# Performance work log

Measured on AMD Instinct MI355X. Metric: run time of the kernel, lower is better.

Reference implementation:

```python
import jax, jax.numpy as jnp
import numpy as np
import math

B, L, DIM = 2, 2048, 2048
N_HEADS, N_KV = 16, 4
HD = DIM // N_HEADS          # 128
N_REP = N_HEADS // N_KV      # 4
THETA = 10000.0


def setup_inputs() -> dict:
    key = jax.random.key(0)
    ks = jax.random.split(key, 6)
    x = jax.random.normal(ks[0], (B, L, DIM), dtype=jnp.float32)
    # rotary phasor freqs_cis = exp(i * t * inv_freq), stored as cos/sin
    inv_freq = 1.0 / (THETA ** (jnp.arange(0, HD, 2, dtype=jnp.float32) / HD))  # [HD//2]
    ang = jnp.arange(L, dtype=jnp.float32)[:, None] * inv_freq[None, :]          # [L, HD//2]
    freqs_cos = jnp.cos(ang)
    freqs_sin = jnp.sin(ang)
    s = 0.02
    wq = jax.random.normal(ks[1], (DIM, DIM), dtype=jnp.float32) * s
    wk = jax.random.normal(ks[2], (N_KV * HD, DIM), dtype=jnp.float32) * s
    wv = jax.random.normal(ks[3], (N_KV * HD, DIM), dtype=jnp.float32) * s
    wo = jax.random.normal(ks[4], (DIM, DIM), dtype=jnp.float32) * s
    return {"x": x, "freqs_cos": freqs_cos, "freqs_sin": freqs_sin,
            "wq": wq, "wk": wk, "wv": wv, "wo": wo}


def _apply_rope(t, cos, sin):
    # t: [B, L, H, HD]; cos/sin: [L, HD//2] -> broadcast [1, L, 1, HD//2]
    tr = t.reshape(*t.shape[:-1], HD // 2, 2)
    t0, t1 = tr[..., 0], tr[..., 1]
    c = cos[None, :, None, :]
    s = sin[None, :, None, :]
    r0 = t0 * c - t1 * s
    r1 = t0 * s + t1 * c
    return jnp.stack([r0, r1], axis=-1).reshape(t.shape)


def reference(x, freqs_cos, freqs_sin, wq, wk, wv, wo):
    Bx, Lx, _ = x.shape
    xq = (x @ wq.T).reshape(Bx, Lx, N_HEADS, HD)
    xk = (x @ wk.T).reshape(Bx, Lx, N_KV, HD)
    xv = (x @ wv.T).reshape(Bx, Lx, N_KV, HD)
    xq = _apply_rope(xq, freqs_cos, freqs_sin)
    xk = _apply_rope(xk, freqs_cos, freqs_sin)
    # repeat_kv (GQA expansion) then [B, H, L, HD]
    keys = jnp.repeat(xk, N_REP, axis=2).transpose(0, 2, 1, 3)
    values = jnp.repeat(xv, N_REP, axis=2).transpose(0, 2, 1, 3)
    q = xq.transpose(0, 2, 1, 3)
    scores = jnp.einsum('bhqd,bhkd->bhqk', q, keys) / math.sqrt(HD)
    mask = jnp.triu(jnp.full((Lx, Lx), -jnp.inf, dtype=scores.dtype), k=1)
    scores = scores + mask[None, None]
    probs = jax.nn.softmax(scores.astype(jnp.float32), axis=-1).astype(q.dtype)
    out = jnp.einsum('bhqk,bhkd->bhqd', probs, values)
    out = out.transpose(0, 2, 1, 3).reshape(Bx, Lx, -1)
    output = out @ wo.T
    return (output, keys, values)
```

## Files before the change

kernel.cpp:

```cpp
#include <hip/hip_runtime.h>
#include <hip/hip_bf16.h>

using bf16x8 = __attribute__((ext_vector_type(8))) short;
using f32x4  = __attribute__((ext_vector_type(4))) float;

__device__ __forceinline__ unsigned short f32_to_bf16(float f) {
  unsigned u = __float_as_uint(f);
  u += 0x7FFFu + ((u >> 16) & 1u);
  return (unsigned short)(u >> 16);
}
__device__ __forceinline__ unsigned pack2(float lo, float hi) {
  __hip_bfloat162 h = __float22bfloat162_rn(make_float2(lo, hi));
  return *reinterpret_cast<unsigned*>(&h);
}
__device__ __forceinline__ void gload_lds16(const void* g, void* l) {
  __builtin_amdgcn_global_load_lds(
      (const __attribute__((address_space(1))) unsigned int*)g,
      (__attribute__((address_space(3))) unsigned int*)l, 16, 0, 0);
}

__global__ void cast_all_kernel(const float* __restrict__ wq, const float* __restrict__ wo,
                                const float* __restrict__ wk, const float* __restrict__ wv,
                                const float* __restrict__ x,
                                unsigned short* __restrict__ WQKV,
                                unsigned short* __restrict__ WO,
                                unsigned short* __restrict__ XBF) {
  int i = blockIdx.x * blockDim.x + threadIdx.x;
  const float4* s; ushort4* d; int j;
  if (i < 1048576)      { s = (const float4*)wq; d = (ushort4*)WQKV;            j = i; }
  else if (i < 2097152) { s = (const float4*)wo; d = (ushort4*)WO;              j = i - 1048576; }
  else if (i < 2359296) { s = (const float4*)wk; d = (ushort4*)WQKV + 1048576;  j = i - 2097152; }
  else if (i < 2621440) { s = (const float4*)wv; d = (ushort4*)WQKV + 1310720;  j = i - 2359296; }
  else                  { s = (const float4*)x;  d = (ushort4*)XBF;             j = i - 2621440; }
  float4 v = s[j];
  ushort4 o;
  o.x = f32_to_bf16(v.x); o.y = f32_to_bf16(v.y);
  o.z = f32_to_bf16(v.z); o.w = f32_to_bf16(v.w);
  d[j] = o;
}

template <int BM, int MODE>
__global__ __launch_bounds__(512, 2) void gemm256_kernel(
    const unsigned short* __restrict__ A, const unsigned short* __restrict__ Bw,
    float* __restrict__ C, unsigned short* __restrict__ qbf_out,
    float* __restrict__ xkv_out, int M, int N, int K) {
  constexpr int ABYTES = BM * 128;
  constexpr int BBYTES = 256 * 128;
  constexpr int BUFB   = ABYTES + BBYTES;
  constexpr int ALOADS = BM / 64;
  constexpr int WROWS  = BM / 32;
  __shared__ __align__(16) char Lsh[2 * BUFB];

  const int tid = threadIdx.x;
  const int wid = tid >> 6, lane = tid & 63;
  const int lr = lane & 15, lg = lane >> 4;
  const int wr = wid >> 2, wc = wid & 3;
  const int bn = blockIdx.x, bm = blockIdx.y;
  const int x0 = lg * 16;

  f32x4 acc[WROWS][4] = {};

  const char* Ag = (const char*)A + (size_t)(bm * BM) * K * 2;
  const char* Bg = (const char*)Bw + (size_t)(bn * 256) * K * 2;

  int aoff[ALOADS], boff[4];
#pragma unroll
  for (int i = 0; i < ALOADS; ++i) {
    int lin = wid * (BM * 16) + i * 1024 + lane * 16;
    int grow = lin >> 7;
    int gcol = (lin & 127) ^ ((grow & 7) << 4);
    aoff[i] = grow * (K * 2) + gcol;
  }
#pragma unroll
  for (int i = 0; i < 4; ++i) {
    int lin = wid * 4096 + i * 1024 + lane * 16;
    int grow = lin >> 7;
    int gcol = (lin & 127) ^ ((grow & 7) << 4);
    boff[i] = grow * (K * 2) + gcol;
  }

  auto stage = [&](int s, int buf) {
    const int kb = s * 128;
    char* Lb = Lsh + buf * BUFB;
#pragma unroll
    for (int i = 0; i < ALOADS; ++i)
      gload_lds16(Ag + aoff[i] + kb, Lb + wid * (BM * 16) + i * 1024);
#pragma unroll
    for (int i = 0; i < 4; ++i)
      gload_lds16(Bg + boff[i] + kb, Lb + ABYTES + wid * 4096 + i * 1024);
  };

  auto kstep = [&](char* Lb) {
    bf16x8 bfr[4][2];
#pragma unroll
    for (int fc = 0; fc < 4; ++fc) {
      const int row = wc * 64 + fc * 16 + lr;
      const int base = ABYTES + row * 128;
      const int sw = (row & 7) << 4;
#pragma unroll
      for (int ks = 0; ks < 2; ++ks)
        bfr[fc][ks] = *reinterpret_cast<const bf16x8*>(Lb + base + ((ks * 64 + x0) ^ sw));
    }
#pragma unroll
    for (int q = 0; q < WROWS / 2; ++q) {
      bf16x8 af[2][2];
#pragma unroll
      for (int t = 0; t < 2; ++t) {
        const int row = wr * (BM / 2) + (2 * q + t) * 16 + lr;
        const int base = row * 128;
        const int sw = (row & 7) << 4;
#pragma unroll
        for (int ks = 0; ks < 2; ++ks)
          af[t][ks] = *reinterpret_cast<const bf16x8*>(Lb + base + ((ks * 64 + x0) ^ sw));
      }
      asm volatile("s_waitcnt lgkmcnt(0)" ::: "memory");
      __builtin_amdgcn_sched_barrier(0);
      __builtin_amdgcn_s_setprio(1);
#pragma unroll
      for (int t = 0; t < 2; ++t)
#pragma unroll
        for (int fc = 0; fc < 4; ++fc) {
          acc[2 * q + t][fc] = __builtin_amdgcn_mfma_f32_16x16x32_bf16(af[t][0], bfr[fc][0], acc[2 * q + t][fc], 0, 0, 0);
          acc[2 * q + t][fc] = __builtin_amdgcn_mfma_f32_16x16x32_bf16(af[t][1], bfr[fc][1], acc[2 * q + t][fc], 0, 0, 0);
        }
      __builtin_amdgcn_s_setprio(0);
    }
  };

  const int NST = K >> 6;
  stage(0, 0);
  for (int it = 0; it < NST / 2; ++it) {
    __builtin_amdgcn_s_barrier();
    stage(2 * it + 1, 1);
    if constexpr (BM == 256) asm volatile("s_waitcnt vmcnt(8)" ::: "memory");
    else                     asm volatile("s_waitcnt vmcnt(6)" ::: "memory");
    __builtin_amdgcn_s_barrier();
    kstep(Lsh);
    __builtin_amdgcn_s_barrier();
    if (it < NST / 2 - 1) {
      stage(2 * it + 2, 0);
      if constexpr (BM == 256) asm volatile("s_waitcnt vmcnt(8)" ::: "memory");
      else                     asm volatile("s_waitcnt vmcnt(6)" ::: "memory");
    } else {
      asm volatile("s_waitcnt vmcnt(0)" ::: "memory");
    }
    __builtin_amdgcn_s_barrier();
    kstep(Lsh + BUFB);
  }

  if constexpr (MODE == 0) {
#pragma unroll
    for (int fr = 0; fr < WROWS; ++fr) {
      const int m = bm * BM + wr * (BM / 2) + fr * 16 + lg * 4;
#pragma unroll
      for (int fc = 0; fc < 4; ++fc) {
        const int n = bn * 256 + wc * 64 + fc * 16 + lr;
#pragma unroll
        for (int r = 0; r < 4; ++r)
          C[(size_t)(m + r) * N + n] = acc[fr][fc][r];
      }
    }
  } else {
    if (bn < 8) {
#pragma unroll
      for (int fr = 0; fr < WROWS; ++fr) {
        const int m = bm * BM + wr * (BM / 2) + fr * 16 + lg * 4;
#pragma unroll
        for (int fc = 0; fc < 4; ++fc) {
          const int n = bn * 256 + wc * 64 + fc * 16 + lr;
#pragma unroll
          for (int r = 0; r < 4; ++r)
            qbf_out[(size_t)(m + r) * 2048 + n] = f32_to_bf16(acc[fr][fc][r]);
        }
      }
    } else {
#pragma unroll
      for (int fr = 0; fr < WROWS; ++fr) {
        const int m = bm * BM + wr * (BM / 2) + fr * 16 + lg * 4;
#pragma unroll
        for (int fc = 0; fc < 4; ++fc) {
          const int n = bn * 256 + wc * 64 + fc * 16 + lr - 2048;
#pragma unroll
          for (int r = 0; r < 4; ++r)
            xkv_out[(size_t)(m + r) * 1024 + n] = acc[fr][fc][r];
        }
      }
    }
  }
}

__global__ void kv_proc_kernel(const float* __restrict__ xkv, const float* __restrict__ fc,
                               const float* __restrict__ fs, unsigned short* __restrict__ kbf,
                               float* __restrict__ keys, unsigned short* __restrict__ vt,
                               float* __restrict__ values) {
  int bid = blockIdx.x;
  if (bid < 4096) {
    int idx = bid * 256 + threadIdx.x;
    int i = idx & 63;
    int kvh = (idx >> 6) & 3;
    int l = (idx >> 8) & 2047;
    int b = idx >> 19;
    float2 t = reinterpret_cast<const float2*>(xkv)[(size_t)(b * 2048 + l) * 512 + kvh * 64 + i];
    float c = fc[l * 64 + i], s = fs[l * 64 + i];
    float r0 = t.x * c - t.y * s;
    float r1 = t.x * s + t.y * c;
    int kidx = ((b * 4 + kvh) * 2048 + l) * 64 + i;
    ushort2 o; o.x = f32_to_bf16(r0); o.y = f32_to_bf16(r1);
    reinterpret_cast<ushort2*>(kbf)[kidx] = o;
    float2 f; f.x = r0; f.y = r1;
#pragma unroll
    for (int rep = 0; rep < 4; ++rep) {
      int h = kvh * 4 + rep;
      reinterpret_cast<float2*>(keys)[((b * 16 + h) * 2048 + l) * 64 + i] = f;
    }
  } else {
    int idx = (bid - 4096) * 256 + threadIdx.x;
    int d = idx & 127;
    int kvh = (idx >> 7) & 3;
    int l = (idx >> 9) & 2047;
    int b = idx >> 20;
    float v = xkv[(size_t)(b * 2048 + l) * 1024 + 512 + kvh * 128 + d];
#pragma unroll
    for (int rep = 0; rep < 4; ++rep) {
      int h = kvh * 4 + rep;
      values[((size_t)(b * 16 + h) * 2048 + l) * 128 + d] = v;
    }
    vt[((size_t)(b * 4 + kvh) * 128 + d) * 2048 + l] = f32_to_bf16(v);
  }
}

__global__ __launch_bounds__(256) void attn_kernel(
    const unsigned short* __restrict__ qbf, const float* __restrict__ fc,
    const float* __restrict__ fs, const unsigned short* __restrict__ kbf,
    const unsigned short* __restrict__ vt, unsigned short* __restrict__ obf) {
  __shared__ unsigned short Ks[64 * 128];
  __shared__ unsigned short Vs[128 * 64];
  __shared__ unsigned short Ps[4][2][16 * 72];
  const int tid = threadIdx.x;
  const int w = tid >> 6, lane = tid & 63;
  const int lr = lane & 15, lg = lane >> 4;
  const int bid = blockIdx.x;
  const int qt = 15 - (bid >> 5);
  const int bh = bid & 31;
  const int b = bh >> 4, h = bh & 15, kv = h >> 2;
  const int q0 = qt * 128 + w * 32;
  const float ALPHA = 0.08838834764831845f;
  const int swz = (lr & 7) << 4;

  bf16x8 qf[2][4];
#pragma unroll
  for (int t = 0; t < 2; ++t) {
    const int qrow = q0 + t * 16 + lr;
    const unsigned short* xqp = qbf + (size_t)(b * 2048 + qrow) * 2048 + h * 128;
    const float* fcp = fc + qrow * 64;
    const float* fsp = fs + qrow * 64;
#pragma unroll
    for (int s = 0; s < 4; ++s) {
      union { bf16x8 v8; unsigned short us[8]; } rw;
      rw.v8 = *reinterpret_cast<const bf16x8*>(xqp + s * 32 + lg * 8);
      float xv[8];
#pragma unroll
      for (int k = 0; k < 8; ++k) xv[k] = __uint_as_float(((unsigned)rw.us[k]) << 16);
      float4 c4 = *reinterpret_cast<const float4*>(fcp + s * 16 + lg * 4);
      float4 s4 = *reinterpret_cast<const float4*>(fsp + s * 16 + lg * 4);
      c4.x *= ALPHA; c4.y *= ALPHA; c4.z *= ALPHA; c4.w *= ALPHA;
      s4.x *= ALPHA; s4.y *= ALPHA; s4.z *= ALPHA; s4.w *= ALPHA;
      union { bf16x8 v8; unsigned u[4]; } uu;
      uu.u[0] = pack2(xv[0] * c4.x - xv[1] * s4.x, xv[0] * s4.x + xv[1] * c4.x);
      uu.u[1] = pack2(xv[2] * c4.y - xv[3] * s4.y, xv[2] * s4.y + xv[3] * c4.y);
      uu.u[2] = pack2(xv[4] * c4.z - xv[5] * s4.z, xv[4] * s4.z + xv[5] * c4.z);
      uu.u[3] = pack2(xv[6] * c4.w - xv[7] * s4.w, xv[6] * s4.w + xv[7] * c4.w);
      qf[t][s] = uu.v8;
    }
  }

  f32x4 acc[2][8] = {};
  float mrow[2] = {-1e30f, -1e30f}, lsum[2] = {0.f, 0.f};

  const char* kgbase = (const char*)(kbf + (size_t)(b * 4 + kv) * 2048 * 128);
  const char* vgbase = (const char*)(vt + (size_t)(b * 4 + kv) * 128 * 2048);

  const int nblocks = 2 * qt + 2;
  for (int j = 0; j < nblocks; ++j) {
    const int kb = j * 64;
    __syncthreads();
#pragma unroll
    for (int i = 0; i < 4; ++i) {
      int p = w * 4096 + i * 1024 + lane * 16;
      int krow = p >> 8;
      int kcol = (p & 255) ^ ((krow & 7) << 4);
      gload_lds16(kgbase + (size_t)(kb + krow) * 256 + kcol, (char*)Ks + w * 4096 + i * 1024);
      int drow = p >> 7;
      int dcol = (p & 127) ^ ((drow & 7) << 4);
      gload_lds16(vgbase + (size_t)drow * 4096 + (size_t)kb * 2 + dcol, (char*)Vs + w * 4096 + i * 1024);
    }
    __syncthreads();
    if (j == nblocks - 1 && w < 2) continue;
    f32x4 sT[2][4];
#pragma unroll
    for (int c = 0; c < 4; ++c) {
      bf16x8 kf[4];
#pragma unroll
      for (int s = 0; s < 4; ++s)
        kf[s] = *reinterpret_cast<const bf16x8*>((char*)Ks + (((c * 16 + lr) * 256 + s * 64 + lg * 16) ^ swz));
      f32x4 t0 = {0.f, 0.f, 0.f, 0.f}, t1 = {0.f, 0.f, 0.f, 0.f};
#pragma unroll
      for (int s = 0; s < 4; ++s) {
        t0 = __builtin_amdgcn_mfma_f32_16x16x32_bf16(kf[s], qf[0][s], t0, 0, 0, 0);
        t1 = __builtin_amdgcn_mfma_f32_16x16x32_bf16(kf[s], qf[1][s], t1, 0, 0, 0);
      }
      sT[0][c] = t0; sT[1][c] = t1;
    }
#pragma unroll
    for (int t = 0; t < 2; ++t) {
      const int qrow = q0 + t * 16 + lr;
      float x[4][4];
      float mt = -1e30f;
#pragma unroll
      for (int c = 0; c < 4; ++c)
#pragma unroll
        for (int r = 0; r < 4; ++r) {
          int k = kb + c * 16 + lg * 4 + r;
          float v = (k <= qrow) ? sT[t][c][r] : -1e30f;
          x[c][r] = v;
          mt = fmaxf(mt, v);
        }
      mt = fmaxf(mt, __shfl_xor(mt, 16));
      mt = fmaxf(mt, __shfl_xor(mt, 32));
      const bool skip = __all(mt <= mrow[t] + 8.0f);
      float mnew, fac;
      if (skip) {
        mnew = mrow[t];
      } else {
        mnew = fmaxf(mrow[t], mt);
        fac = __expf(mrow[t] - mnew);
        mrow[t] = mnew;
      }
      float rs = 0.f;
      unsigned pw[4][2];
#pragma unroll
      for (int c = 0; c < 4; ++c)
#pragma unroll
        for (int j2 = 0; j2 < 2; ++j2) {
          float p0 = __expf(x[c][2 * j2] - mnew);
          float p1 = __expf(x[c][2 * j2 + 1] - mnew);
          rs += p0 + p1;
          pw[c][j2] = pack2(p0, p1);
        }
      rs += __shfl_xor(rs, 16);
      rs += __shfl_xor(rs, 32);
      if (skip) {
        lsum[t] += rs;
      } else {
        lsum[t] = lsum[t] * fac + rs;
#pragma unroll
        for (int dt = 0; dt < 8; ++dt)
#pragma unroll
          for (int r = 0; r < 4; ++r) acc[t][dt][r] *= fac;
      }
      char* pb = (char*)&Ps[w][t][0];
#pragma unroll
      for (int c = 0; c < 4; ++c)
#pragma unroll
        for (int j2 = 0; j2 < 2; ++j2)
          *reinterpret_cast<unsigned*>(pb + lr * 144 + c * 32 + lg * 8 + j2 * 4) = pw[c][j2];
    }
    asm volatile("s_waitcnt lgkmcnt(0)" ::: "memory");
    __builtin_amdgcn_sched_barrier(0);
    bf16x8 pt[2][2];
#pragma unroll
    for (int t = 0; t < 2; ++t)
#pragma unroll
      for (int kk = 0; kk < 2; ++kk)
        pt[t][kk] = *reinterpret_cast<const bf16x8*>((char*)&Ps[w][t][0] + lr * 144 + kk * 64 + lg * 16);
#pragma unroll
    for (int dt = 0; dt < 8; ++dt) {
      bf16x8 v0 = *reinterpret_cast<const bf16x8*>((char*)Vs + (((dt * 16 + lr) * 128 + lg * 16) ^ swz));
      bf16x8 v1 = *reinterpret_cast<const bf16x8*>((char*)Vs + (((dt * 16 + lr) * 128 + 64 + lg * 16) ^ swz));
      acc[0][dt] = __builtin_amdgcn_mfma_f32_16x16x32_bf16(v0, pt[0][0], acc[0][dt], 0, 0, 0);
      acc[0][dt] = __builtin_amdgcn_mfma_f32_16x16x32_bf16(v1, pt[0][1], acc[0][dt], 0, 0, 0);
      acc[1][dt] = __builtin_amdgcn_mfma_f32_16x16x32_bf16(v0, pt[1][0], acc[1][dt], 0, 0, 0);
      acc[1][dt] = __builtin_amdgcn_mfma_f32_16x16x32_bf16(v1, pt[1][1], acc[1][dt], 0, 0, 0);
    }
  }
#pragma unroll
  for (int t = 0; t < 2; ++t) {
    float inv = 1.0f / lsum[t];
#pragma unroll
    for (int dt = 0; dt < 8; ++dt) {
      ushort4 o;
      o.x = f32_to_bf16(acc[t][dt][0] * inv);
      o.y = f32_to_bf16(acc[t][dt][1] * inv);
      o.z = f32_to_bf16(acc[t][dt][2] * inv);
      o.w = f32_to_bf16(acc[t][dt][3] * inv);
      *reinterpret_cast<ushort4*>(obf + ((size_t)(b * 2048 + q0 + t * 16 + lr)) * 2048 + h * 128 + dt * 16 + lg * 4) = o;
    }
  }
}

extern "C" void kernel_launch(void* const* d_in, const int* in_sizes, int n_in,
                              void* d_out, int out_size, void* d_ws, size_t ws_size,
                              hipStream_t stream) {
  const float* x  = (const float*)d_in[0];
  const float* fc = (const float*)d_in[1];
  const float* fs = (const float*)d_in[2];
  const float* wq = (const float*)d_in[3];
  const float* wk = (const float*)d_in[4];
  const float* wv = (const float*)d_in[5];
  const float* wo = (const float*)d_in[6];

  float* out    = (float*)d_out;
  float* keys   = out + 8388608;
  float* values = out + 16777216;

  char* ws = (char*)d_ws;
  unsigned short* WQKV = (unsigned short*)(ws + 0);
  unsigned short* WO   = (unsigned short*)(ws + 12582912);
  unsigned short* XBF  = (unsigned short*)(ws + 20971520);
  unsigned short* QBF  = (unsigned short*)(ws + 37748736);
  float*          XKV  = (float*)(ws + 54525952);
  unsigned short* KBF  = (unsigned short*)(ws + 88080384);
  unsigned short* VTB  = (unsigned short*)(ws + 92274688);
  unsigned short* ATT  = XBF;

  cast_all_kernel<<<18432, 256, 0, stream>>>(wq, wo, wk, wv, x, WQKV, WO, XBF);

  gemm256_kernel<256, 1><<<dim3(12, 16), 512, 0, stream>>>(
      XBF, WQKV, nullptr, QBF, XKV, 4096, 3072, 2048);

  kv_proc_kernel<<<12288, 256, 0, stream>>>(XKV, fc, fs, KBF, keys, VTB, values);

  attn_kernel<<<512, 256, 0, stream>>>(QBF, fc, fs, KBF, VTB, ATT);

  gemm256_kernel<128, 0><<<dim3(8, 32), 512, 0, stream>>>(
      ATT, WO, out, nullptr, nullptr, 4096, 2048, 2048);
}
```

Measured before the change: 223.1 us.

## Permute K rows at load so P stays in registers, dropping LDS round-trip

Loads K tile rows into shared memory in a permuted order. This makes the QK^T MFMA output layout match the B-operand layout needed for the PV MFMA, so softmax probabilities are packed directly in registers instead of being written to and read back from an LDS scratch buffer with a waitcnt. The causal mask index is recomputed for the permuted key order. Global load address offsets are also precomputed outside the key loop. The risk is mask or permutation errors, plus somewhat different global access coalescing for K loads.

Result: no change. 222.7 us (median of 2 runs) (-0.2%).

```diff
diff --git a/kernel.cpp b/kernel.cpp
--- a/kernel.cpp
+++ b/kernel.cpp
@@ -235,7 +235,6 @@
     const unsigned short* __restrict__ vt, unsigned short* __restrict__ obf) {
   __shared__ unsigned short Ks[64 * 128];
   __shared__ unsigned short Vs[128 * 64];
-  __shared__ unsigned short Ps[4][2][16 * 72];
   const int tid = threadIdx.x;
   const int w = tid >> 6, lane = tid & 63;
   const int lr = lane & 15, lg = lane >> 4;
@@ -280,19 +279,27 @@
   const char* kgbase = (const char*)(kbf + (size_t)(b * 4 + kv) * 2048 * 128);
   const char* vgbase = (const char*)(vt + (size_t)(b * 4 + kv) * 128 * 2048);
 
+  int ksrc[4], vsrc[4];
+#pragma unroll
+  for (int i = 0; i < 4; ++i) {
+    int p = w * 4096 + i * 1024 + lane * 16;
+    int krow = p >> 8;
+    int kperm = ((krow >> 5) << 5) + ((krow >> 4) & 1) + (((krow >> 2) & 3) << 3) + ((krow & 3) << 1);
+    int kcol = (p & 255) ^ ((krow & 7) << 4);
+    ksrc[i] = kperm * 256 + kcol;
+    int drow = p >> 7;
+    int dcol = (p & 127) ^ ((drow & 7) << 4);
+    vsrc[i] = drow * 4096 + dcol;
+  }
+
   const int nblocks = 2 * qt + 2;
   for (int j = 0; j < nblocks; ++j) {
     const int kb = j * 64;
     __syncthreads();
 #pragma unroll
     for (int i = 0; i < 4; ++i) {
-      int p = w * 4096 + i * 1024 + lane * 16;
-      int krow = p >> 8;
-      int kcol = (p & 255) ^ ((krow & 7) << 4);
-      gload_lds16(kgbase + (size_t)(kb + krow) * 256 + kcol, (char*)Ks + w * 4096 + i * 1024);
-      int drow = p >> 7;
-      int dcol = (p & 127) ^ ((drow & 7) << 4);
-      gload_lds16(vgbase + (size_t)drow * 4096 + (size_t)kb * 2 + dcol, (char*)Vs + w * 4096 + i * 1024);
+      gload_lds16(kgbase + (size_t)kb * 256 + ksrc[i], (char*)Ks + w * 4096 + i * 1024);
+      gload_lds16(vgbase + (size_t)kb * 2 + vsrc[i], (char*)Vs + w * 4096 + i * 1024);
     }
     __syncthreads();
     if (j == nblocks - 1 && w < 2) continue;
@@ -311,6 +318,7 @@
       }
       sT[0][c] = t0; sT[1][c] = t1;
     }
+    bf16x8 ptf[2][2];
 #pragma unroll
     for (int t = 0; t < 2; ++t) {
       const int qrow = q0 + t * 16 + lr;
@@ -320,8 +328,8 @@
       for (int c = 0; c < 4; ++c)
 #pragma unroll
         for (int r = 0; r < 4; ++r) {
-          int k = kb + c * 16 + lg * 4 + r;
-          float v = (k <= qrow) ? sT[t][c][r] : -1e30f;
+          int ka = kb + ((c >> 1) << 5) + (c & 1) + 8 * lg + 2 * r;
+          float v = (ka <= qrow) ? sT[t][c][r] : -1e30f;
           x[c][r] = v;
           mt = fmaxf(mt, v);
         }
@@ -337,15 +345,14 @@
         mrow[t] = mnew;
       }
       float rs = 0.f;
-      unsigned pw[4][2];
+      float pv[4][4];
 #pragma unroll
       for (int c = 0; c < 4; ++c)
 #pragma unroll
-        for (int j2 = 0; j2 < 2; ++j2) {
-          float p0 = __expf(x[c][2 * j2] - mnew);
-          float p1 = __expf(x[c][2 * j2 + 1] - mnew);
-          rs += p0 + p1;
-          pw[c][j2] = pack2(p0, p1);
+        for (int r = 0; r < 4; ++r) {
+          float p = __expf(x[c][r] - mnew);
+          pv[c][r] = p;
+          rs += p;
         }
       rs += __shfl_xor(rs, 16);
       rs += __shfl_xor(rs, 32);
@@ -358,29 +365,23 @@
 #pragma unroll
           for (int r = 0; r < 4; ++r) acc[t][dt][r] *= fac;
       }
-      char* pb = (char*)&Ps[w][t][0];
-#pragma unroll
-      for (int c = 0; c < 4; ++c)
-#pragma unroll
-        for (int j2 = 0; j2 < 2; ++j2)
-          *reinterpret_cast<unsigned*>(pb + lr * 144 + c * 32 + lg * 8 + j2 * 4) = pw[c][j2];
-    }
-    asm volatile("s_waitcnt lgkmcnt(0)" ::: "memory");
-    __builtin_amdgcn_sched_barrier(0);
-    bf16x8 pt[2][2];
-#pragma unroll
-    for (int t = 0; t < 2; ++t)
-#pragma unroll
-      for (int kk = 0; kk < 2; ++kk)
-        pt[t][kk] = *reinterpret_cast<const bf16x8*>((char*)&Ps[w][t][0] + lr * 144 + kk * 64 + lg * 16);
+#pragma unroll
+      for (int kk = 0; kk < 2; ++kk) {
+        union { bf16x8 v8; unsigned u[4]; } uu;
+#pragma unroll
+        for (int wd = 0; wd < 4; ++wd)
+          uu.u[wd] = pack2(pv[2 * kk][wd], pv[2 * kk + 1][wd]);
+        ptf[t][kk] = uu.v8;
+      }
+    }
 #pragma unroll
     for (int dt = 0; dt < 8; ++dt) {
       bf16x8 v0 = *reinterpret_cast<const bf16x8*>((char*)Vs + (((dt * 16 + lr) * 128 + lg * 16) ^ swz));
       bf16x8 v1 = *reinterpret_cast<const bf16x8*>((char*)Vs + (((dt * 16 + lr) * 128 + 64 + lg * 16) ^ swz));
-      acc[0][dt] = __builtin_amdgcn_mfma_f32_16x16x32_bf16(v0, pt[0][0], acc[0][dt], 0, 0, 0);
-      acc[0][dt] = __builtin_amdgcn_mfma_f32_16x16x32_bf16(v1, pt[0][1], acc[0][dt], 0, 0, 0);
-      acc[1][dt] = __builtin_amdgcn_mfma_f32_16x16x32_bf16(v0, pt[1][0], acc[1][dt], 0, 0, 0);
-      acc[1][dt] = __builtin_amdgcn_mfma_f32_16x16x32_bf16(v1, pt[1][1], acc[1][dt], 0, 0, 0);
+      acc[0][dt] = __builtin_amdgcn_mfma_f32_16x16x32_bf16(v0, ptf[0][0], acc[0][dt], 0, 0, 0);
+      acc[0][dt] = __builtin_amdgcn_mfma_f32_16x16x32_bf16(v1, ptf[0][1], acc[0][dt], 0, 0, 0);
+      acc[1][dt] = __builtin_amdgcn_mfma_f32_16x16x32_bf16(v0, ptf[1][0], acc[1][dt], 0, 0, 0);
+      acc[1][dt] = __builtin_amdgcn_mfma_f32_16x16x32_bf16(v1, ptf[1][1], acc[1][dt], 0, 0, 0);
     }
   }
 #pragma unroll
```
